# Kernel optimization log

Measured on AMD Instinct MI355X. Metric: run time of the kernel, lower is better.

## Reference

```python
import jax, jax.numpy as jnp
import numpy as np

NF, NV = 200000, 100000
C_IN, MULT, K = 128, 2, 16
C_OUT = 128
BN_EPS = 1e-3


def setup_inputs() -> dict:
    key = jax.random.key(0)
    ks = jax.random.split(key, 8)
    inputs = jax.random.normal(ks[0], (NF, C_IN), dtype=jnp.float32)
    filt_coeff = jax.random.uniform(ks[1], (NF, K), dtype=jnp.float32)
    face = jax.random.randint(ks[2], (NF, 3), 0, NV, dtype=jnp.int32)
    nf_count = jax.random.randint(ks[3], (NV,), 0, 12, dtype=jnp.int32)
    vt_map = jnp.arange(NV, dtype=jnp.int32)
    # parameters (xavier-normal-like init for weights)
    sw_std = float(np.sqrt(2.0 / (C_IN + MULT)))
    spatial_weights = jax.random.normal(ks[4], (K, C_IN, MULT), dtype=jnp.float32) * sw_std
    dw_std = float(np.sqrt(2.0 / (C_IN * MULT + C_OUT)))
    depth_weights = jax.random.normal(ks[5], (C_IN * MULT, C_OUT), dtype=jnp.float32) * dw_std
    biases = jnp.zeros((1, C_OUT), dtype=jnp.float32)
    gamma = jnp.ones((C_OUT,), dtype=jnp.float32)
    beta = jnp.zeros((C_OUT,), dtype=jnp.float32)
    return {"inputs": inputs, "filt_coeff": filt_coeff, "face": face,
            "nf_count": nf_count, "vt_map": vt_map,
            "spatial_weights": spatial_weights, "depth_weights": depth_weights,
            "biases": biases, "gamma": gamma, "beta": beta}


def reference(inputs, filt_coeff, face, nf_count, vt_map,
              spatial_weights, depth_weights, biases, gamma, beta):
    Nf, C = inputs.shape
    Kb, _, M = spatial_weights.shape
    Nv = nf_count.shape[0]
    # per-face mixture kernel:  w[f,c,m] = sum_k filt_coeff[f,k] * spatial_weights[k,c,m]
    w = jnp.einsum('fk,kcm->fcm', filt_coeff, spatial_weights)
    feat = (inputs[:, :, None] * w).reshape(Nf, C * M)  # [Nf, C*M]
    # scatter facet features to the 3 incident vertices (mapped via vt_map)
    tgt = vt_map[face]  # [Nf, 3]
    agg = jnp.zeros((Nv, C * M), dtype=feat.dtype)
    for j in range(3):  # small fixed structural loop (3 verts per triangle)
        agg = agg + jax.ops.segment_sum(feat, tgt[:, j], num_segments=Nv)
    denom = jnp.maximum(nf_count, 1).astype(feat.dtype)[:, None]
    vert = agg / denom  # mean over incident facets, [Nv, C*M]
    # dense depthwise (pointwise) matmul + bias + ReLU
    out = vert @ depth_weights + biases
    out = jax.nn.relu(out)
    # BatchNorm1d (training-mode batch statistics, eps=1e-3)
    mean = out.mean(axis=0)
    var = out.var(axis=0)
    out = (out - mean) * jax.lax.rsqrt(var + BN_EPS) * gamma + beta
    return out
```

## Files before the change

### kernel.cpp

```cpp
#include <hip/hip_runtime.h>
#include <hip/hip_bf16.h>


constexpr int C_IN  = 128;
constexpr int KF    = 16;
constexpr int CM    = 256;
constexpr int C_OUT = 128;
constexpr int CAP   = 32;
constexpr int GB    = 1024;
constexpr int FT    = 64;
constexpr int GRIDF = 512;
constexpr float BN_EPS = 1e-3f;

typedef __attribute__((ext_vector_type(8))) short short8;
typedef __attribute__((ext_vector_type(4))) float f32x4;

__device__ __forceinline__ ushort f2bf(float x) {
  union { float f; unsigned u; } v; v.f = x;
  return (ushort)((v.u + 0x7fffu + ((v.u >> 16) & 1u)) >> 16);
}
__device__ __forceinline__ float b2f(ushort u) {
  return __uint_as_float((unsigned)u << 16);
}
__device__ __forceinline__ uint pk2(float a, float b) {
  __hip_bfloat162 h = __float22bfloat162_rn(float2{a, b});
  return *(uint*)&h;
}
__device__ __forceinline__ void dma16(const float* g, void* l) {
  __builtin_amdgcn_global_load_lds(
      (const __attribute__((address_space(1))) void*)g,
      (__attribute__((address_space(3))) void*)l, 16, 0, 0);
}
__device__ __forceinline__ void bar_raw() {
  __builtin_amdgcn_s_barrier();
  asm volatile("" ::: "memory");
}
__device__ __forceinline__ void bar_lds() {
  asm volatile("s_waitcnt lgkmcnt(0)" ::: "memory");
  __builtin_amdgcn_s_barrier();
  asm volatile("" ::: "memory");
}

__global__ __launch_bounds__(256) void k_prepfill(
    const float* __restrict__ dw, const float* __restrict__ sw,
    ushort* __restrict__ dwt, ushort* __restrict__ swt,
    const int* __restrict__ face, const int* __restrict__ vt_map,
    int* __restrict__ cnt, int* __restrict__ slots, int n_inc) {
  const int b = blockIdx.x, tid = threadIdx.x;
  if (b < 64) {
    int i = b * 512 + tid;
#pragma unroll
    for (int r = 0; r < 2; ++r, i += 256) {
      int n = i >> 8, k = i & 255;
      dwt[i] = f2bf(dw[k * C_OUT + n]);
    }
  } else if (b < 96) {
    int i = (b - 64) * 256 + tid;
    int cm = i >> 5, k = i & 31;
    swt[i] = (k < KF) ? f2bf(sw[k * CM + cm]) : (ushort)0;
  } else {
    int i = (b - 96) * 256 + tid;
    if (i < n_inc) {
      int f = i / 3;
      int v = vt_map[face[i]];
      int p = atomicAdd(&cnt[v], 1);
      if (p < CAP) slots[(size_t)v * CAP + p] = f;
    }
  }
}

__global__ __launch_bounds__(256, 2) void k_faceg(
    const float* __restrict__ inp, const float* __restrict__ fc,
    const ushort* __restrict__ swt, const ushort* __restrict__ dwt,
    ushort* __restrict__ g, int ntiles) {
  __shared__ __align__(1024) ushort s_buf[2][FT * 256];

  const int tid  = threadIdx.x;
  const int w    = tid >> 6;
  const int lane = tid & 63;
  const int rm   = lane & 15;
  const int kg   = lane >> 4;

  short8 a1[4];
#pragma unroll
  for (int ct = 0; ct < 4; ++ct)
    a1[ct] = *(const short8*)&swt[(size_t)(w * 64 + ct * 16 + rm) * 32 + kg * 8];
  short8 bfr[2][8];
#pragma unroll
  for (int nt = 0; nt < 2; ++nt) {
    const int n = (w * 2 + nt) * 16 + rm;
#pragma unroll
    for (int ks = 0; ks < 8; ++ks)
      bfr[nt][ks] = *(const short8*)&dwt[n * 256 + ks * 32 + kg * 8];
  }

  auto issue_dma = [&](int buf, int fb) {
#pragma unroll
    for (int it = 0; it < 8; ++it) {
      const int row   = w * 16 + it * 2 + (lane >> 5);
      const int chunk = lane & 31;
      const float* src = inp + (size_t)(fb + row) * C_IN + ((chunk ^ (row & 7)) << 2);
      dma16(src, (char*)s_buf + buf * 32768 + w * 8192 + it * 1024);
    }
  };

  int t = blockIdx.x;
  issue_dma(0, t * FT);
  int cur = 0;

  for (; t < ntiles; t += GRIDF, cur ^= 1) {
    const int fb = t * FT;
    char* sb = (char*)s_buf + cur * 32768;

    bar_lds();

    float4 p0[4], p1[4];
#pragma unroll
    for (int ft = 0; ft < 4; ++ft) {
      const float* fr = &fc[(size_t)(fb + ft * 16 + rm) * KF + (kg & 1) * 8];
      p0[ft] = *(const float4*)fr;
      p1[ft] = *(const float4*)(fr + 4);
    }

    const int tn = t + GRIDF;
    if (tn < ntiles) {
      issue_dma(cur ^ 1, tn * FT);
      asm volatile("s_waitcnt vmcnt(8)" ::: "memory");
    } else {
      asm volatile("s_waitcnt vmcnt(0)" ::: "memory");
    }

    short8 b1[4];
#pragma unroll
    for (int ft = 0; ft < 4; ++ft) {
      uint4 u;
      u.x = pk2(p0[ft].x, p0[ft].y); u.y = pk2(p0[ft].z, p0[ft].w);
      u.z = pk2(p1[ft].x, p1[ft].y); u.w = pk2(p1[ft].z, p1[ft].w);
      if (kg >= 2) u = uint4{0, 0, 0, 0};
      b1[ft] = *(short8*)&u;
    }

    bar_raw();

#pragma unroll
    for (int ft = 0; ft < 4; ++ft) {
#pragma unroll
      for (int ct = 0; ct < 4; ++ct) {
        f32x4 acc = {0.f, 0.f, 0.f, 0.f};
        acc = __builtin_amdgcn_mfma_f32_16x16x32_bf16(a1[ct], b1[ft], acc, 0, 0, 0);
        const int face = ft * 16 + rm;
        const int cmb  = w * 64 + ct * 16 + kg * 4;
        const int byt  = face * 512 + ((((cmb * 2) >> 4) ^ (face & 7)) << 4)
                       + ((cmb * 2) & 15);
        const float2 ivv = *(const float2*)(sb + byt);
        uint2 pw;
        pw.x = pk2(acc[0] * ivv.x, acc[1] * ivv.x);
        pw.y = pk2(acc[2] * ivv.y, acc[3] * ivv.y);
        *(uint2*)(sb + byt) = pw;
      }
    }

    bar_lds();

    f32x4 acc2[4][2];
#pragma unroll
    for (int fs = 0; fs < 4; ++fs)
#pragma unroll
      for (int nt = 0; nt < 2; ++nt)
        acc2[fs][nt] = (f32x4){0.f, 0.f, 0.f, 0.f};

#pragma unroll
    for (int fs = 0; fs < 4; ++fs)
#pragma unroll
      for (int ks = 0; ks < 8; ++ks) {
        const int row = fs * 16 + rm;
        const int byt = row * 512 + (((ks * 4 + kg) ^ (row & 7)) << 4);
        const short8 af = *(const short8*)(sb + byt);
        acc2[fs][0] = __builtin_amdgcn_mfma_f32_16x16x32_bf16(af, bfr[0][ks], acc2[fs][0], 0, 0, 0);
        acc2[fs][1] = __builtin_amdgcn_mfma_f32_16x16x32_bf16(af, bfr[1][ks], acc2[fs][1], 0, 0, 0);
      }

    bar_lds();

#pragma unroll
    for (int fs = 0; fs < 4; ++fs)
#pragma unroll
      for (int nt = 0; nt < 2; ++nt)
#pragma unroll
        for (int r = 0; r < 4; ++r) {
          const int row = fs * 16 + kg * 4 + r;
          const int col = (w * 2 + nt) * 16 + rm;
          const int byt = row * 512 + (((col >> 2) ^ (row & 7)) << 4) + (col & 3) * 4;
          *(float*)(sb + byt) = acc2[fs][nt][r];
        }

    bar_lds();

    const int irow = tid >> 2;
    const int q    = tid & 3;
#pragma unroll
    for (int i = 0; i < 4; ++i) {
      const int c0 = 2 * q + 8 * i;
      const float4 a = *(const float4*)(sb + irow * 512 + ((c0 ^ (irow & 7)) << 4));
      const float4 b = *(const float4*)(sb + irow * 512 + (((c0 + 1) ^ (irow & 7)) << 4));
      uint4 u;
      u.x = pk2(a.x, a.y); u.y = pk2(a.z, a.w);
      u.z = pk2(b.x, b.y); u.w = pk2(b.z, b.w);
      *(short8*)&g[(size_t)(fb + irow) * C_OUT + c0 * 4] = *(short8*)&u;
    }
  }
}

__global__ __launch_bounds__(256) void k_gather(
    const ushort* __restrict__ g, const int* __restrict__ cnt,
    const int* __restrict__ slots, const int* __restrict__ nf_cnt,
    const float* __restrict__ bias, ushort* __restrict__ pre,
    float* __restrict__ part, int nv, int ntiles) {
  __shared__ float s_red[256][8];

  const int tid = threadIdx.x;
  const int q   = tid & 15;
  const int vg  = tid >> 4;
  const int c8  = q * 8;

  float bs[8];
#pragma unroll
  for (int j = 0; j < 8; ++j) bs[j] = bias[c8 + j];
  float st_s[8], st_q[8];
#pragma unroll
  for (int j = 0; j < 8; ++j) { st_s[j] = 0.f; st_q[j] = 0.f; }

  for (int tile = blockIdx.x; tile < ntiles; tile += gridDim.x) {
    const int v = tile * 16 + vg;
    int deg = cnt[v]; deg = deg > CAP ? CAP : deg;
    const int* sl = &slots[(size_t)v * CAP];

    float a[8];
#pragma unroll
    for (int j = 0; j < 8; ++j) a[j] = 0.f;

    int t = 0;
    for (; t + 4 <= deg; t += 4) {
      const int4 ff = *(const int4*)&sl[t];
      const short8 r0 = *(const short8*)&g[(size_t)ff.x * C_OUT + c8];
      const short8 r1 = *(const short8*)&g[(size_t)ff.y * C_OUT + c8];
      const short8 r2 = *(const short8*)&g[(size_t)ff.z * C_OUT + c8];
      const short8 r3 = *(const short8*)&g[(size_t)ff.w * C_OUT + c8];
#pragma unroll
      for (int j = 0; j < 8; ++j)
        a[j] += (b2f((ushort)r0[j]) + b2f((ushort)r1[j]))
              + (b2f((ushort)r2[j]) + b2f((ushort)r3[j]));
    }
    for (; t < deg; ++t) {
      const short8 r0 = *(const short8*)&g[(size_t)sl[t] * C_OUT + c8];
#pragma unroll
      for (int j = 0; j < 8; ++j) a[j] += b2f((ushort)r0[j]);
    }

    int d = nf_cnt[v]; if (d < 1) d = 1;
    const float inv = 1.0f / (float)d;
    float r[8];
#pragma unroll
    for (int j = 0; j < 8; ++j) {
      r[j] = fmaxf(fmaf(a[j], inv, bs[j]), 0.f);
      st_s[j] += r[j];
      st_q[j] = fmaf(r[j], r[j], st_q[j]);
    }
    uint4 u;
    u.x = pk2(r[0], r[1]); u.y = pk2(r[2], r[3]);
    u.z = pk2(r[4], r[5]); u.w = pk2(r[6], r[7]);
    *(short8*)&pre[(size_t)v * C_OUT + c8] = *(short8*)&u;
  }

#pragma unroll
  for (int j = 0; j < 8; ++j) s_red[tid][j] = st_s[j];
  __syncthreads();
  if (tid < 16) {
    for (int j = 0; j < 8; ++j) {
      float x = 0.f;
      for (int gg = 0; gg < 16; ++gg) x += s_red[gg * 16 + tid][j];
      part[(size_t)(tid * 8 + j) * GB + blockIdx.x] = x;
    }
  }
  __syncthreads();
#pragma unroll
  for (int j = 0; j < 8; ++j) s_red[tid][j] = st_q[j];
  __syncthreads();
  if (tid < 16) {
    for (int j = 0; j < 8; ++j) {
      float x = 0.f;
      for (int gg = 0; gg < 16; ++gg) x += s_red[gg * 16 + tid][j];
      part[(size_t)(128 + tid * 8 + j) * GB + blockIdx.x] = x;
    }
  }
}

__global__ __launch_bounds__(256) void k_red(const float* __restrict__ part,
                                             float* __restrict__ red) {
  const int j   = blockIdx.x;
  const int tid = threadIdx.x;
  float v = 0.f;
#pragma unroll
  for (int b = 0; b < GB; b += 256) v += part[(size_t)j * GB + b + tid];
#pragma unroll
  for (int off = 32; off > 0; off >>= 1) v += __shfl_down(v, off);
  __shared__ float sred[4];
  if ((tid & 63) == 0) sred[tid >> 6] = v;
  __syncthreads();
  if (tid == 0) red[j] = sred[0] + sred[1] + sred[2] + sred[3];
}

__global__ void k_fin(const float* __restrict__ red,
                      const float* __restrict__ gamma, const float* __restrict__ beta,
                      float* __restrict__ scale, float* __restrict__ shift, float invN) {
  int o = threadIdx.x;
  float mean = red[o] * invN;
  float var  = red[128 + o] * invN - mean * mean;
  float sc   = gamma[o] * rsqrtf(var + BN_EPS);
  scale[o] = sc;
  shift[o] = fmaf(-mean, sc, beta[o]);
}

__global__ __launch_bounds__(256) void k_bn(const ushort* __restrict__ pre,
                                            const float* __restrict__ scale,
                                            const float* __restrict__ shift,
                                            float* __restrict__ out, int n8) {
  int idx = blockIdx.x * blockDim.x + threadIdx.x;
  const int stride = gridDim.x * blockDim.x;
  for (; idx < n8; idx += stride) {
    const short8 pv = *(const short8*)&pre[(size_t)idx * 8];
    const int base = (idx * 8) & (C_OUT - 1);
    const float4 sc0 = *(const float4*)&scale[base];
    const float4 sc1 = *(const float4*)&scale[base + 4];
    const float4 sh0 = *(const float4*)&shift[base];
    const float4 sh1 = *(const float4*)&shift[base + 4];
    float4 o0, o1;
    o0.x = fmaf(b2f((ushort)pv[0]), sc0.x, sh0.x);
    o0.y = fmaf(b2f((ushort)pv[1]), sc0.y, sh0.y);
    o0.z = fmaf(b2f((ushort)pv[2]), sc0.z, sh0.z);
    o0.w = fmaf(b2f((ushort)pv[3]), sc0.w, sh0.w);
    o1.x = fmaf(b2f((ushort)pv[4]), sc1.x, sh1.x);
    o1.y = fmaf(b2f((ushort)pv[5]), sc1.y, sh1.y);
    o1.z = fmaf(b2f((ushort)pv[6]), sc1.z, sh1.z);
    o1.w = fmaf(b2f((ushort)pv[7]), sc1.w, sh1.w);
    *(float4*)&out[(size_t)idx * 8]     = o0;
    *(float4*)&out[(size_t)idx * 8 + 4] = o1;
  }
}

extern "C" void kernel_launch(void* const* d_in, const int* in_sizes, int n_in,
                              void* d_out, int out_size, void* d_ws, size_t ws_size,
                              hipStream_t stream) {
  const float* inputs = (const float*)d_in[0];
  const float* fc     = (const float*)d_in[1];
  const int*   face   = (const int*)d_in[2];
  const int*   nf_cnt = (const int*)d_in[3];
  const int*   vt_map = (const int*)d_in[4];
  const float* sw     = (const float*)d_in[5];
  const float* dw     = (const float*)d_in[6];
  const float* bias   = (const float*)d_in[7];
  const float* gamma  = (const float*)d_in[8];
  const float* beta   = (const float*)d_in[9];
  float* out = (float*)d_out;

  const int nf = in_sizes[0] / C_IN;
  const int nv = in_sizes[3];

  char* p = (char*)d_ws;
  int*    cnt   = (int*)p;            p += (size_t)nv * 4;
  float*  scale = (float*)p;          p += C_OUT * 4;
  float*  shift = (float*)p;          p += C_OUT * 4;
  float*  red   = (float*)p;          p += 256 * 4;
  float*  part  = (float*)p;          p += (size_t)256 * GB * 4;
  ushort* dwt   = (ushort*)p;         p += (size_t)C_OUT * CM * 2;
  ushort* swt   = (ushort*)p;         p += (size_t)CM * 32 * 2;
  int*    slots = (int*)p;            p += (size_t)nv * CAP * 4;
  ushort* g     = (ushort*)p;         p += (size_t)nf * C_OUT * 2;
  ushort* pre   = (ushort*)p;

  hipMemsetAsync(cnt, 0, (size_t)nv * 4, stream);

  const int n_inc = nf * 3;
  const int fill_blocks = (n_inc + 255) / 256;
  k_prepfill<<<96 + fill_blocks, 256, 0, stream>>>(dw, sw, dwt, swt,
                                                   face, vt_map, cnt, slots, n_inc);

  const int ntiles_f = (nf + FT - 1) / FT;
  k_faceg<<<GRIDF, 256, 0, stream>>>(inputs, fc, swt, dwt, g, ntiles_f);

  const int ntiles_v = (nv + 15) / 16;
  k_gather<<<GB, 256, 0, stream>>>(g, cnt, slots, nf_cnt, bias, pre, part, nv, ntiles_v);

  k_red<<<256, 256, 0, stream>>>(part, red);
  k_fin<<<1, 128, 0, stream>>>(red, gamma, beta, scale, shift, 1.0f / (float)nv);

  const int n8 = (nv * C_OUT) / 8;
  k_bn<<<2048, 256, 0, stream>>>(pre, scale, shift, out, n8);
}
```

Baseline: 135.6 us.

## Make face-tile pipeline wave-private to drop block barriers in k_faceg

Each wave now owns 16 faces of the 64-face tile, with its own double-buffered LDS region. Block-wide s_barriers become per-wave waitcnt fences, so waves no longer stall on each other. Each wave keeps all 16 spatial-weight fragments in registers and streams the depthwise weight fragments from global memory every tile instead of keeping them resident. The trade is more global/L2 traffic per tile and a full vmcnt(0) wait at each loop top, which also waits on outstanding stores, in exchange for removing the inter-wave syncs.

```diff
diff --git a/kernel.cpp b/kernel.cpp
--- a/kernel.cpp
+++ b/kernel.cpp
@@ -31,14 +31,13 @@
       (const __attribute__((address_space(1))) void*)g,
       (__attribute__((address_space(3))) void*)l, 16, 0, 0);
 }
-__device__ __forceinline__ void bar_raw() {
-  __builtin_amdgcn_s_barrier();
-  asm volatile("" ::: "memory");
-}
-__device__ __forceinline__ void bar_lds() {
+__device__ __forceinline__ void fence_lds() {
   asm volatile("s_waitcnt lgkmcnt(0)" ::: "memory");
-  __builtin_amdgcn_s_barrier();
-  asm volatile("" ::: "memory");
+  __builtin_amdgcn_sched_barrier(0);
+}
+__device__ __forceinline__ void fence_vm() {
+  asm volatile("s_waitcnt vmcnt(0)" ::: "memory");
+  __builtin_amdgcn_sched_barrier(0);
 }
 
 __global__ __launch_bounds__(256) void k_prepfill(
@@ -73,7 +72,7 @@
     const float* __restrict__ inp, const float* __restrict__ fc,
     const ushort* __restrict__ swt, const ushort* __restrict__ dwt,
     ushort* __restrict__ g, int ntiles) {
-  __shared__ __align__(1024) ushort s_buf[2][FT * 256];
+  __shared__ __align__(1024) char s_lds[4][2][8192];
 
   const int tid  = threadIdx.x;
   const int w    = tid >> 6;
@@ -81,26 +80,21 @@
   const int rm   = lane & 15;
   const int kg   = lane >> 4;
 
-  short8 a1[4];
-#pragma unroll
-  for (int ct = 0; ct < 4; ++ct)
-    a1[ct] = *(const short8*)&swt[(size_t)(w * 64 + ct * 16 + rm) * 32 + kg * 8];
-  short8 bfr[2][8];
-#pragma unroll
-  for (int nt = 0; nt < 2; ++nt) {
-    const int n = (w * 2 + nt) * 16 + rm;
-#pragma unroll
-    for (int ks = 0; ks < 8; ++ks)
-      bfr[nt][ks] = *(const short8*)&dwt[n * 256 + ks * 32 + kg * 8];
-  }
+  char* wbase = &s_lds[w][0][0];
+
+  short8 a1[16];
+#pragma unroll
+  for (int ct = 0; ct < 16; ++ct)
+    a1[ct] = *(const short8*)&swt[(size_t)(ct * 16 + rm) * 32 + kg * 8];
 
   auto issue_dma = [&](int buf, int fb) {
 #pragma unroll
     for (int it = 0; it < 8; ++it) {
-      const int row   = w * 16 + it * 2 + (lane >> 5);
+      const int row   = it * 2 + (lane >> 5);
       const int chunk = lane & 31;
-      const float* src = inp + (size_t)(fb + row) * C_IN + ((chunk ^ (row & 7)) << 2);
-      dma16(src, (char*)s_buf + buf * 32768 + w * 8192 + it * 1024);
+      const float* src = inp + (size_t)(fb + w * 16 + row) * C_IN
+                       + ((chunk ^ (row & 7)) << 2);
+      dma16(src, wbase + buf * 8192 + it * 1024);
     }
   };
 
@@ -110,103 +104,84 @@
 
   for (; t < ntiles; t += GRIDF, cur ^= 1) {
     const int fb = t * FT;
-    char* sb = (char*)s_buf + cur * 32768;
-
-    bar_lds();
-
-    float4 p0[4], p1[4];
-#pragma unroll
-    for (int ft = 0; ft < 4; ++ft) {
-      const float* fr = &fc[(size_t)(fb + ft * 16 + rm) * KF + (kg & 1) * 8];
-      p0[ft] = *(const float4*)fr;
-      p1[ft] = *(const float4*)(fr + 4);
-    }
+    char* sb = wbase + cur * 8192;
+
+    fence_vm();
+
+    const float* fr = &fc[(size_t)(fb + w * 16 + rm) * KF + (kg & 1) * 8];
+    const float4 p0 = *(const float4*)fr;
+    const float4 p1 = *(const float4*)(fr + 4);
 
     const int tn = t + GRIDF;
-    if (tn < ntiles) {
-      issue_dma(cur ^ 1, tn * FT);
-      asm volatile("s_waitcnt vmcnt(8)" ::: "memory");
-    } else {
-      asm volatile("s_waitcnt vmcnt(0)" ::: "memory");
-    }
-
-    short8 b1[4];
-#pragma unroll
-    for (int ft = 0; ft < 4; ++ft) {
+    if (tn < ntiles) issue_dma(cur ^ 1, tn * FT);
+
+    short8 b1;
+    {
       uint4 u;
-      u.x = pk2(p0[ft].x, p0[ft].y); u.y = pk2(p0[ft].z, p0[ft].w);
-      u.z = pk2(p1[ft].x, p1[ft].y); u.w = pk2(p1[ft].z, p1[ft].w);
+      u.x = pk2(p0.x, p0.y); u.y = pk2(p0.z, p0.w);
+      u.z = pk2(p1.x, p1.y); u.w = pk2(p1.z, p1.w);
       if (kg >= 2) u = uint4{0, 0, 0, 0};
-      b1[ft] = *(short8*)&u;
-    }
-
-    bar_raw();
-
-#pragma unroll
-    for (int ft = 0; ft < 4; ++ft) {
-#pragma unroll
-      for (int ct = 0; ct < 4; ++ct) {
-        f32x4 acc = {0.f, 0.f, 0.f, 0.f};
-        acc = __builtin_amdgcn_mfma_f32_16x16x32_bf16(a1[ct], b1[ft], acc, 0, 0, 0);
-        const int face = ft * 16 + rm;
-        const int cmb  = w * 64 + ct * 16 + kg * 4;
-        const int byt  = face * 512 + ((((cmb * 2) >> 4) ^ (face & 7)) << 4)
-                       + ((cmb * 2) & 15);
-        const float2 ivv = *(const float2*)(sb + byt);
-        uint2 pw;
-        pw.x = pk2(acc[0] * ivv.x, acc[1] * ivv.x);
-        pw.y = pk2(acc[2] * ivv.y, acc[3] * ivv.y);
-        *(uint2*)(sb + byt) = pw;
+      b1 = *(short8*)&u;
+    }
+
+#pragma unroll
+    for (int ct = 0; ct < 16; ++ct) {
+      f32x4 acc = {0.f, 0.f, 0.f, 0.f};
+      acc = __builtin_amdgcn_mfma_f32_16x16x32_bf16(a1[ct], b1, acc, 0, 0, 0);
+      const int face = rm;
+      const int cmb  = ct * 16 + kg * 4;
+      const int byt  = face * 512 + ((((cmb * 2) >> 4) ^ (face & 7)) << 4)
+                     + ((cmb * 2) & 15);
+      const float2 ivv = *(const float2*)(sb + byt);
+      uint2 pw;
+      pw.x = pk2(acc[0] * ivv.x, acc[1] * ivv.x);
+      pw.y = pk2(acc[2] * ivv.y, acc[3] * ivv.y);
+      *(uint2*)(sb + byt) = pw;
+    }
+
+    fence_lds();
+
+    short8 af[8];
+#pragma unroll
+    for (int ks = 0; ks < 8; ++ks) {
+      const int byt = rm * 512 + (((ks * 4 + kg) ^ (rm & 7)) << 4);
+      af[ks] = *(const short8*)(sb + byt);
+    }
+    fence_lds();
+
+#pragma unroll
+    for (int nt = 0; nt < 8; ++nt) {
+      short8 bfr[8];
+#pragma unroll
+      for (int ks = 0; ks < 8; ++ks)
+        bfr[ks] = *(const short8*)&dwt[(nt * 16 + rm) * 256 + ks * 32 + kg * 8];
+      f32x4 acc = {0.f, 0.f, 0.f, 0.f};
+#pragma unroll
+      for (int ks = 0; ks < 8; ++ks)
+        acc = __builtin_amdgcn_mfma_f32_16x16x32_bf16(af[ks], bfr[ks], acc, 0, 0, 0);
+#pragma unroll
+      for (int r = 0; r < 4; ++r) {
+        const int face = kg * 4 + r;
+        const int col  = nt * 16 + rm;
+        const int byt  = face * 512 + (((col >> 2) ^ (face & 7)) << 4)
+                       + (col & 3) * 4;
+        *(float*)(sb + byt) = acc[r];
       }
     }
 
-    bar_lds();
-
-    f32x4 acc2[4][2];
-#pragma unroll
-    for (int fs = 0; fs < 4; ++fs)
-#pragma unroll
-      for (int nt = 0; nt < 2; ++nt)
-        acc2[fs][nt] = (f32x4){0.f, 0.f, 0.f, 0.f};
-
-#pragma unroll
-    for (int fs = 0; fs < 4; ++fs)
-#pragma unroll
-      for (int ks = 0; ks < 8; ++ks) {
-        const int row = fs * 16 + rm;
-        const int byt = row * 512 + (((ks * 4 + kg) ^ (row & 7)) << 4);
-        const short8 af = *(const short8*)(sb + byt);
-        acc2[fs][0] = __builtin_amdgcn_mfma_f32_16x16x32_bf16(af, bfr[0][ks], acc2[fs][0], 0, 0, 0);
-        acc2[fs][1] = __builtin_amdgcn_mfma_f32_16x16x32_bf16(af, bfr[1][ks], acc2[fs][1], 0, 0, 0);
-      }
-
-    bar_lds();
-
-#pragma unroll
-    for (int fs = 0; fs < 4; ++fs)
-#pragma unroll
-      for (int nt = 0; nt < 2; ++nt)
-#pragma unroll
-        for (int r = 0; r < 4; ++r) {
-          const int row = fs * 16 + kg * 4 + r;
-          const int col = (w * 2 + nt) * 16 + rm;
-          const int byt = row * 512 + (((col >> 2) ^ (row & 7)) << 4) + (col & 3) * 4;
-          *(float*)(sb + byt) = acc2[fs][nt][r];
-        }
-
-    bar_lds();
-
-    const int irow = tid >> 2;
-    const int q    = tid & 3;
+    fence_lds();
+
+    const int row = lane >> 2;
+    const int q   = lane & 3;
 #pragma unroll
     for (int i = 0; i < 4; ++i) {
       const int c0 = 2 * q + 8 * i;
-      const float4 a = *(const float4*)(sb + irow * 512 + ((c0 ^ (irow & 7)) << 4));
-      const float4 b = *(const float4*)(sb + irow * 512 + (((c0 + 1) ^ (irow & 7)) << 4));
+      const float4 a = *(const float4*)(sb + row * 512 + ((c0 ^ (row & 7)) << 4));
+      const float4 b = *(const float4*)(sb + row * 512 + (((c0 + 1) ^ (row & 7)) << 4));
       uint4 u;
       u.x = pk2(a.x, a.y); u.y = pk2(a.z, a.w);
       u.z = pk2(b.x, b.y); u.w = pk2(b.z, b.w);
-      *(short8*)&g[(size_t)(fb + irow) * C_OUT + c0 * 4] = *(short8*)&u;
+      *(short8*)&g[(size_t)(fb + w * 16 + row) * C_OUT + c0 * 4] = *(short8*)&u;
     }
   }
 }
```

Measured after the change: 291.4 us. 115% more time.
